# Kernel optimization log

Measured on AMD Instinct MI355X. Metric: run time of the kernel, lower is better.

Reference implementation:

```python
import jax, jax.numpy as jnp
import numpy as np

N, H, E, C, V, K = 4096, 256, 128, 32, 64, 20


def setup_inputs() -> dict:
    key = jax.random.key(0)
    ks = jax.random.split(key, 16)
    f = lambda k, s: jax.random.normal(k, s, dtype=jnp.float32)
    return {
        "vec": f(ks[0], (N, H)),
        "inp": f(ks[1], (N, E)),
        "h_prev": f(ks[2], (N, H)),
        "c_prev": f(ks[3], (N, H)),
        "Wlin": f(ks[4], (C, V, H)) * 0.05,
        "blin": f(ks[5], (C, V)) * 0.05,
        "Wec": f(ks[6], (2, H)) * 0.05,
        "bec": f(ks[7], (2,)) * 0.05,
        "Wrel": f(ks[8], (5, H)) * 0.05,
        "brel": f(ks[9], (5,)) * 0.05,
        "W_ih": f(ks[10], (K, 4 * H, E)) * 0.05,
        "b_ih": f(ks[11], (K, 4 * H)) * 0.05,
        "W_hh": f(ks[12], (K, 4 * H, H)) * 0.05,
        "b_hh": f(ks[13], (K, 4 * H)) * 0.05,
        "category": jax.random.randint(ks[14], (N,), 0, C, dtype=jnp.int32),
        "cell_id": jax.random.randint(ks[15], (N,), 0, K, dtype=jnp.int32),
        "true_idx": jax.random.randint(jax.random.fold_in(key, 100), (N,), 0, V, dtype=jnp.int32),
        "ec_idx": jax.random.randint(jax.random.fold_in(key, 101), (N,), 0, 2, dtype=jnp.int32),
        "rel_idx": jax.random.randint(jax.random.fold_in(key, 102), (N,), 0, 5, dtype=jnp.int32),
    }


def _ce(logits, targets):
    # per-row cross entropy (same math as nn.CrossEntropyLoss per example)
    logp = jax.nn.log_softmax(logits, axis=-1)
    return -jnp.take_along_axis(logp, targets[:, None], axis=-1)[:, 0]


def reference(vec, inp, h_prev, c_prev, Wlin, blin, Wec, bec, Wrel, brel,
              W_ih, b_ih, W_hh, b_hh, category, cell_id, true_idx, ec_idx, rel_idx):
    # --- get_log_odds: per-category tiny linear head, selected by category ---
    logits_all = jnp.einsum('nh,cvh->ncv', vec, Wlin) + blin          # [N,C,V]
    logits = jnp.take_along_axis(logits_all, category[:, None, None].astype(jnp.int32), axis=1)[:, 0]  # [N,V]
    logits_ec = vec @ Wec.T + bec                                      # [N,2]
    logits_rel = vec @ Wrel.T + brel                                   # [N,5]

    # --- calculate_loss: CE over valid children + ec + rel ---
    losses = _ce(logits, true_idx) + _ce(logits_ec, ec_idx) + _ce(logits_rel, rel_idx)  # [N]

    # --- get_next: per-child-index LSTMCell, selected by cell_id ---
    gates_all = (jnp.einsum('ne,kge->nkg', inp, W_ih)
                 + jnp.einsum('nh,kgh->nkg', h_prev, W_hh)
                 + b_ih + b_hh)                                        # [N,K,4H]
    gates = jnp.take_along_axis(gates_all, cell_id[:, None, None].astype(jnp.int32), axis=1)[:, 0]  # [N,4H]
    i, f, g, o = jnp.split(gates, 4, axis=-1)                          # torch LSTMCell gate order i,f,g,o
    c_next = jax.nn.sigmoid(f) * c_prev + jax.nn.sigmoid(i) * jnp.tanh(g)
    h_next = jax.nn.sigmoid(o) * jnp.tanh(c_next)

    # pack: [N, 1 + 2H] = loss | h_next | c_next
    return jnp.concatenate([losses[:, None], h_next, c_next], axis=-1)
```

## Files before the change

### kernel.cpp

```cpp
#include <hip/hip_runtime.h>
#include <hip/hip_bf16.h>
#include <math.h>

#define Nn 4096
#define Hdim 256
#define Edim 128
#define Cdim 32
#define Vdim 64
#define Kdim 20
#define G4H 1024
#define OUTS 513

#define NB 8
#define LMAX 160
#define MAXG (NB * LMAX)
#define MAXT2 192
#define GRID (MAXG + MAXT2)

typedef short bf16x8 __attribute__((ext_vector_type(8)));
typedef float f32x4 __attribute__((ext_vector_type(4)));

__device__ __forceinline__ float sigmoidf_(float x) { return 1.0f / (1.0f + expf(-x)); }

__device__ __forceinline__ bf16x8 cvt8(float4 f0, float4 f1) {
    bf16x8 r;
    __hip_bfloat16 h;
    h = __float2bfloat16(f0.x); r[0] = *(short*)&h;
    h = __float2bfloat16(f0.y); r[1] = *(short*)&h;
    h = __float2bfloat16(f0.z); r[2] = *(short*)&h;
    h = __float2bfloat16(f0.w); r[3] = *(short*)&h;
    h = __float2bfloat16(f1.x); r[4] = *(short*)&h;
    h = __float2bfloat16(f1.y); r[5] = *(short*)&h;
    h = __float2bfloat16(f1.z); r[6] = *(short*)&h;
    h = __float2bfloat16(f1.w); r[7] = *(short*)&h;
    return r;
}

__device__ __forceinline__ void gl_lds16(const float* g, void* l) {
    __builtin_amdgcn_global_load_lds((const __attribute__((address_space(1))) void*)g,
                                     (__attribute__((address_space(3))) void*)l, 16, 0, 0);
}

__global__ __launch_bounds__(256, 4) void k_all(
    const float* __restrict__ vec, const float* __restrict__ inp,
    const float* __restrict__ h_prev, const float* __restrict__ c_prev,
    const float* __restrict__ Wlin, const float* __restrict__ blin,
    const float* __restrict__ Wec, const float* __restrict__ bec,
    const float* __restrict__ Wrel, const float* __restrict__ brel,
    const float* __restrict__ W_ih, const float* __restrict__ b_ih,
    const float* __restrict__ W_hh, const float* __restrict__ b_hh,
    const int* __restrict__ category, const int* __restrict__ cell_id,
    const int* __restrict__ true_idx, const int* __restrict__ ec_idx, const int* __restrict__ rel_idx,
    float* __restrict__ out)
{
    __shared__ __align__(16) char smem[37120];
    int* rows_s = (int*)(smem + 36864);
    int* cnt  = (int*)smem;
    int* scan = (int*)(smem + 128);
    int* map  = (int*)(smem + 1152);

    int t = threadIdx.x;
    bool is_lstm = blockIdx.x < MAXG;
    const int* key = is_lstm ? cell_id : category;
    int nbins = is_lstm ? Kdim : Cdim;
    int nslots = is_lstm ? MAXG : MAXT2;
    int myslot = is_lstm ? blockIdx.x : (blockIdx.x - MAXG);

    if (t < nbins) cnt[t] = 0;
    for (int i = t; i < nslots; i += 256) map[i] = -1;
    __syncthreads();
    for (int i = t; i < Nn; i += 256) atomicAdd(&cnt[key[i]], 1);
    __syncthreads();
    if (is_lstm) {
        if (t < Kdim * 4) {
            int u = t, k = u >> 2, b = u & 7;
            int base = 0;
            for (int v = b; v < u; v += NB) base += (cnt[v >> 2] + 31) >> 5;
            int n = (cnt[k] + 31) >> 5;
            for (int s = 0; s < n; s++) {
                int slot = (base + s) * NB + b;
                if (slot < MAXG) map[slot] = u | (s << 8);
            }
        }
    } else {
        if (t < Cdim) {
            int m = t;
            int base = 0;
            for (int mm = 0; mm < m; mm++) base += (cnt[mm] + 31) >> 5;
            int n = (cnt[m] + 31) >> 5;
            for (int s = 0; s < n; s++) {
                int slot = base + s;
                if (slot < MAXT2) map[slot] = m | (s << 8);
            }
        }
    }
    __syncthreads();
    int me = map[myslot];
    if (me < 0) return;
    int myk = (me & 255);
    int s = me >> 8;
    int hb0 = 0;
    if (is_lstm) { hb0 = (myk & 3) * 64; myk >>= 2; }
    int w0 = s * 32;
    int rcount = min(32, cnt[myk] - w0);

    {
        int i0 = t * 16;
        int local = 0;
        for (int i = i0; i < i0 + 16; i++) local += (key[i] == myk) ? 1 : 0;
        scan[t] = local;
        __syncthreads();
        for (int off = 1; off < 256; off <<= 1) {
            int v = scan[t];
            int add = (t >= off) ? scan[t - off] : 0;
            __syncthreads();
            scan[t] = v + add;
            __syncthreads();
        }
        int rank = scan[t] - local;
        for (int i = i0; i < i0 + 16; i++) {
            if (key[i] == myk) {
                if (rank >= w0 && rank < w0 + 32) rows_s[rank - w0] = i;
                rank++;
            }
        }
        __syncthreads();
        if (t < 32 && t >= rcount) rows_s[t] = rows_s[0];
        __syncthreads();
    }

    int w = t >> 6, l = t & 63;
    int l15 = l & 15, quad = l >> 4;
    int lrow8 = l >> 3, lslot = l & 7;
    int swz_l = ((l15 & 3) << 1) | ((l15 >> 2) & 1);
    int p0 = (quad * 2) ^ swz_l;

    if (is_lstm) {
        float* Wbuf = (float*)smem;
        float* Xbuf = (float*)(smem + 32768);
        const float* Wih_k = W_ih + (size_t)myk * G4H * Edim;
        const float* Whh_k = W_hh + (size_t)myk * G4H * Hdim;

        f32x4 acc[2][4];
        #pragma unroll
        for (int m = 0; m < 2; m++)
            #pragma unroll
            for (int g = 0; g < 4; g++)
                acc[m][g] = (f32x4){0.f, 0.f, 0.f, 0.f};

        int xr = w * 8 + lrow8;
        int xrow = rows_s[xr];
        int xg = lslot ^ (((xr & 3) << 1) | ((xr >> 2) & 1));

        for (int st = 0; st < 12; st++) {
            int k0 = st * 32;
            const float* Wsrc; int stride, ko;
            if (k0 < Edim) { Wsrc = Wih_k; stride = Edim; ko = k0; }
            else           { Wsrc = Whh_k; stride = Hdim; ko = k0 - Edim; }
            __syncthreads();
            #pragma unroll
            for (int j = 0; j < 8; j++) {
                int r = w * 64 + j * 8 + lrow8;
                int g = lslot ^ (((r & 3) << 1) | ((r >> 2) & 1));
                int gate = r >> 6, hl = r & 63;
                gl_lds16(Wsrc + (size_t)(gate * Hdim + hb0 + hl) * stride + ko + g * 4,
                         Wbuf + (w * 64 + j * 8) * 32);
            }
            gl_lds16((k0 < Edim ? inp + (size_t)xrow * Edim + ko
                                : h_prev + (size_t)xrow * Hdim + ko) + xg * 4,
                     Xbuf + (w * 8) * 32);
            __syncthreads();

            bf16x8 af[2], bfr[4];
            #pragma unroll
            for (int m = 0; m < 2; m++) {
                int row = m * 16 + l15;
                float4 lo = *(float4*)(Xbuf + row * 32 + p0 * 4);
                float4 hi = *(float4*)(Xbuf + row * 32 + (p0 ^ 1) * 4);
                af[m] = cvt8(lo, hi);
            }
            #pragma unroll
            for (int g = 0; g < 4; g++) {
                int row = g * 64 + w * 16 + l15;
                float4 lo = *(float4*)(Wbuf + row * 32 + p0 * 4);
                float4 hi = *(float4*)(Wbuf + row * 32 + (p0 ^ 1) * 4);
                bfr[g] = cvt8(lo, hi);
            }
            #pragma unroll
            for (int m = 0; m < 2; m++)
                #pragma unroll
                for (int g = 0; g < 4; g++)
                    acc[m][g] = __builtin_amdgcn_mfma_f32_16x16x32_bf16(af[m], bfr[g], acc[m][g], 0, 0, 0);
        }

        int h = hb0 + w * 16 + l15;
        float bs[4];
        #pragma unroll
        for (int g = 0; g < 4; g++)
            bs[g] = b_ih[(size_t)myk * G4H + g * Hdim + h] + b_hh[(size_t)myk * G4H + g * Hdim + h];

        #pragma unroll
        for (int m = 0; m < 2; m++) {
            #pragma unroll
            for (int reg = 0; reg < 4; reg++) {
                int r = m * 16 + quad * 4 + reg;
                if (r < rcount) {
                    int row = rows_s[r];
                    float iv = acc[m][0][reg] + bs[0];
                    float fv = acc[m][1][reg] + bs[1];
                    float gv = acc[m][2][reg] + bs[2];
                    float ov = acc[m][3][reg] + bs[3];
                    float cp = c_prev[(size_t)row * Hdim + h];
                    float cn = sigmoidf_(fv) * cp + sigmoidf_(iv) * tanhf(gv);
                    float hn = sigmoidf_(ov) * tanhf(cn);
                    out[(size_t)row * OUTS + 1 + h] = hn;
                    out[(size_t)row * OUTS + 1 + Hdim + h] = cn;
                }
            }
        }
    } else {
        float* Wlbuf = (float*)smem;
        float* Vbuf  = (float*)(smem + 10240);
        float* Lg    = (float*)(smem + 14336);
        int m2 = myk;

        f32x4 a0[2], a1[2];
        #pragma unroll
        for (int m = 0; m < 2; m++) { a0[m] = (f32x4){0.f,0.f,0.f,0.f}; a1[m] = (f32x4){0.f,0.f,0.f,0.f}; }

        int xr = w * 8 + lrow8;
        int xrow = rows_s[xr];
        int xg = lslot ^ (((xr & 3) << 1) | ((xr >> 2) & 1));

        for (int st = 0; st < 8; st++) {
            int ko = st * 32;
            __syncthreads();
            for (int n = w; n < 10; n += 4) {
                int r = n * 8 + lrow8;
                int g = lslot ^ (((r & 3) << 1) | ((r >> 2) & 1));
                const float* srcW;
                if (r < 64)      srcW = Wlin + ((size_t)m2 * Vdim + r) * Hdim;
                else if (r < 66) srcW = Wec + (size_t)(r - 64) * Hdim;
                else if (r < 71) srcW = Wrel + (size_t)(r - 66) * Hdim;
                else             srcW = Wlin + (size_t)m2 * Vdim * Hdim;
                gl_lds16(srcW + ko + g * 4, Wlbuf + n * 8 * 32);
            }
            gl_lds16(vec + (size_t)xrow * Hdim + ko + xg * 4, Vbuf + (w * 8) * 32);
            __syncthreads();

            bf16x8 af[2];
            #pragma unroll
            for (int m = 0; m < 2; m++) {
                int row = m * 16 + l15;
                float4 lo = *(float4*)(Vbuf + row * 32 + p0 * 4);
                float4 hi = *(float4*)(Vbuf + row * 32 + (p0 ^ 1) * 4);
                af[m] = cvt8(lo, hi);
            }
            {
                int row = w * 16 + l15;
                float4 lo = *(float4*)(Wlbuf + row * 32 + p0 * 4);
                float4 hi = *(float4*)(Wlbuf + row * 32 + (p0 ^ 1) * 4);
                bf16x8 b0 = cvt8(lo, hi);
                a0[0] = __builtin_amdgcn_mfma_f32_16x16x32_bf16(af[0], b0, a0[0], 0, 0, 0);
                a0[1] = __builtin_amdgcn_mfma_f32_16x16x32_bf16(af[1], b0, a0[1], 0, 0, 0);
            }
            if (w == 3) {
                int row = 64 + l15;
                float4 lo = *(float4*)(Wlbuf + row * 32 + p0 * 4);
                float4 hi = *(float4*)(Wlbuf + row * 32 + (p0 ^ 1) * 4);
                bf16x8 b1 = cvt8(lo, hi);
                a1[0] = __builtin_amdgcn_mfma_f32_16x16x32_bf16(af[0], b1, a1[0], 0, 0, 0);
                a1[1] = __builtin_amdgcn_mfma_f32_16x16x32_bf16(af[1], b1, a1[1], 0, 0, 0);
            }
        }
        __syncthreads();
        {
            int col = w * 16 + l15;
            float bb = blin[m2 * Vdim + col];
            #pragma unroll
            for (int m = 0; m < 2; m++)
                #pragma unroll
                for (int reg = 0; reg < 4; reg++)
                    Lg[(m * 16 + quad * 4 + reg) * 84 + col] = a0[m][reg] + bb;
            if (w == 3) {
                int col1 = 64 + l15;
                float bb1 = (l15 < 2) ? bec[l15] : ((l15 < 7) ? brel[l15 - 2] : 0.f);
                #pragma unroll
                for (int m = 0; m < 2; m++)
                    #pragma unroll
                    for (int reg = 0; reg < 4; reg++)
                        Lg[(m * 16 + quad * 4 + reg) * 84 + col1] = a1[m][reg] + bb1;
            }
        }
        __syncthreads();
        for (int rr = 0; rr < 8; rr++) {
            int r = w * 8 + rr;
            if (r >= rcount) break;
            int orig = rows_s[r];
            float lg = Lg[r * 84 + l];
            float mx = lg;
            for (int ss = 32; ss >= 1; ss >>= 1) mx = fmaxf(mx, __shfl_xor(mx, ss));
            float sm = expf(lg - mx);
            for (int ss = 32; ss >= 1; ss >>= 1) sm += __shfl_xor(sm, ss);
            float lt = __shfl(lg, true_idx[orig]);
            float loss = mx + logf(sm) - lt;
            if (l == 0) {
                float l0 = Lg[r * 84 + 64], l1 = Lg[r * 84 + 65];
                float me2 = fmaxf(l0, l1);
                loss += me2 + logf(expf(l0 - me2) + expf(l1 - me2)) - ((ec_idx[orig] == 0) ? l0 : l1);
                float rl[5] = { Lg[r * 84 + 66], Lg[r * 84 + 67], Lg[r * 84 + 68], Lg[r * 84 + 69], Lg[r * 84 + 70] };
                float mr = rl[0];
                #pragma unroll
                for (int i = 1; i < 5; i++) mr = fmaxf(mr, rl[i]);
                float sr = 0.f;
                #pragma unroll
                for (int i = 0; i < 5; i++) sr += expf(rl[i] - mr);
                loss += mr + logf(sr) - rl[rel_idx[orig]];
                out[(size_t)orig * OUTS] = loss;
            }
        }
    }
}

extern "C" void kernel_launch(void* const* d_in, const int* in_sizes, int n_in,
                              void* d_out, int out_size, void* d_ws, size_t ws_size,
                              hipStream_t stream) {
    const float* vec      = (const float*)d_in[0];
    const float* inp      = (const float*)d_in[1];
    const float* h_prev   = (const float*)d_in[2];
    const float* c_prev   = (const float*)d_in[3];
    const float* Wlin     = (const float*)d_in[4];
    const float* blin     = (const float*)d_in[5];
    const float* Wec      = (const float*)d_in[6];
    const float* bec      = (const float*)d_in[7];
    const float* Wrel     = (const float*)d_in[8];
    const float* brel     = (const float*)d_in[9];
    const float* W_ih     = (const float*)d_in[10];
    const float* b_ih     = (const float*)d_in[11];
    const float* W_hh     = (const float*)d_in[12];
    const float* b_hh     = (const float*)d_in[13];
    const int*   category = (const int*)d_in[14];
    const int*   cell_id  = (const int*)d_in[15];
    const int*   true_idx = (const int*)d_in[16];
    const int*   ec_idx   = (const int*)d_in[17];
    const int*   rel_idx  = (const int*)d_in[18];
    float* out = (float*)d_out;

    k_all<<<GRID, 256, 0, stream>>>(
        vec, inp, h_prev, c_prev, Wlin, blin, Wec, bec, Wrel, brel,
        W_ih, b_ih, W_hh, b_hh, category, cell_id, true_idx, ec_idx, rel_idx, out);
}
```

Before: 156.9 us.

## Double LSTM row tile to 64 and streamline per-block binning with register keys

```diff
diff --git a/kernel.cpp b/kernel.cpp
--- a/kernel.cpp
+++ b/kernel.cpp
@@ -12,8 +12,8 @@
 #define OUTS 513
 
 #define NB 8
-#define LMAX 160
-#define MAXG (NB * LMAX)
+#define LMAXL 96
+#define MAXG (NB * LMAXL)
 #define MAXT2 192
 #define GRID (MAXG + MAXT2)
 
@@ -41,6 +41,8 @@
                                      (__attribute__((address_space(3))) void*)l, 16, 0, 0);
 }
 
+__device__ __forceinline__ int swz(int r) { return ((r & 3) << 1) | ((r >> 2) & 1); }
+
 __global__ __launch_bounds__(256, 4) void k_all(
     const float* __restrict__ vec, const float* __restrict__ inp,
     const float* __restrict__ h_prev, const float* __restrict__ c_prev,
@@ -53,86 +55,98 @@
     const int* __restrict__ true_idx, const int* __restrict__ ec_idx, const int* __restrict__ rel_idx,
     float* __restrict__ out)
 {
-    __shared__ __align__(16) char smem[37120];
-    int* rows_s = (int*)(smem + 36864);
-    int* cnt  = (int*)smem;
-    int* scan = (int*)(smem + 128);
-    int* map  = (int*)(smem + 1152);
+    __shared__ __align__(16) char smem[40960];
+    int* cntR = (int*)smem;
+    int* cntF = (int*)(smem + 8192);
+    int* wsum = (int*)(smem + 8320);
+    int* rows_tmp = (int*)(smem + 8448);
 
     int t = threadIdx.x;
+    int w = t >> 6, l = t & 63;
+    int l15 = l & 15, quad = l >> 4;
+    int lrow8 = l >> 3, lslot = l & 7;
     bool is_lstm = blockIdx.x < MAXG;
     const int* key = is_lstm ? cell_id : category;
     int nbins = is_lstm ? Kdim : Cdim;
-    int nslots = is_lstm ? MAXG : MAXT2;
-    int myslot = is_lstm ? blockIdx.x : (blockIdx.x - MAXG);
-
-    if (t < nbins) cnt[t] = 0;
-    for (int i = t; i < nslots; i += 256) map[i] = -1;
+
+    for (int i = t; i < nbins * 16; i += 256) cntR[i] = 0;
     __syncthreads();
-    for (int i = t; i < Nn; i += 256) atomicAdd(&cnt[key[i]], 1);
+    int4 kv0 = ((const int4*)key)[t * 4 + 0];
+    int4 kv1 = ((const int4*)key)[t * 4 + 1];
+    int4 kv2 = ((const int4*)key)[t * 4 + 2];
+    int4 kv3 = ((const int4*)key)[t * 4 + 3];
+    int ks[16] = { kv0.x, kv0.y, kv0.z, kv0.w, kv1.x, kv1.y, kv1.z, kv1.w,
+                   kv2.x, kv2.y, kv2.z, kv2.w, kv3.x, kv3.y, kv3.z, kv3.w };
+    int rep = t & 15;
+    #pragma unroll
+    for (int j = 0; j < 16; j++) atomicAdd(&cntR[ks[j] * 16 + rep], 1);
     __syncthreads();
-    if (is_lstm) {
-        if (t < Kdim * 4) {
-            int u = t, k = u >> 2, b = u & 7;
-            int base = 0;
-            for (int v = b; v < u; v += NB) base += (cnt[v >> 2] + 31) >> 5;
-            int n = (cnt[k] + 31) >> 5;
-            for (int s = 0; s < n; s++) {
-                int slot = (base + s) * NB + b;
-                if (slot < MAXG) map[slot] = u | (s << 8);
-            }
-        }
-    } else {
-        if (t < Cdim) {
-            int m = t;
-            int base = 0;
-            for (int mm = 0; mm < m; mm++) base += (cnt[mm] + 31) >> 5;
-            int n = (cnt[m] + 31) >> 5;
-            for (int s = 0; s < n; s++) {
-                int slot = base + s;
-                if (slot < MAXT2) map[slot] = m | (s << 8);
-            }
-        }
+    if (t < nbins) {
+        int s2 = 0;
+        #pragma unroll
+        for (int r2 = 0; r2 < 16; r2++) s2 += cntR[t * 16 + r2];
+        cntF[t] = s2;
     }
     __syncthreads();
-    int me = map[myslot];
-    if (me < 0) return;
-    int myk = (me & 255);
-    int s = me >> 8;
-    int hb0 = 0;
-    if (is_lstm) { hb0 = (myk & 3) * 64; myk >>= 2; }
-    int w0 = s * 32;
-    int rcount = min(32, cnt[myk] - w0);
+
+    int myk, s_idx, hb0 = 0, rcount, wlen;
+    if (is_lstm) {
+        int b = blockIdx.x & 7, pos = blockIdx.x >> 3;
+        int u = -1, sf = 0, acc = 0;
+        for (int uu = b; uu < Kdim * 4; uu += NB) {
+            int n = (cntF[uu >> 2] + 63) >> 6;
+            if (u < 0 && pos < acc + n) { u = uu; sf = pos - acc; }
+            acc += n;
+        }
+        if (u < 0) return;
+        myk = u >> 2; hb0 = (u & 3) * 64; s_idx = sf;
+        wlen = 64;
+        rcount = min(64, cntF[myk] - s_idx * 64);
+    } else {
+        int slot = blockIdx.x - MAXG;
+        int u = -1, sf = 0, acc = 0;
+        for (int m = 0; m < Cdim; m++) {
+            int n = (cntF[m] + 31) >> 5;
+            if (u < 0 && slot < acc + n) { u = m; sf = slot - acc; }
+            acc += n;
+        }
+        if (u < 0) return;
+        myk = u; s_idx = sf;
+        wlen = 32;
+        rcount = min(32, cntF[myk] - s_idx * 32);
+    }
 
     {
-        int i0 = t * 16;
         int local = 0;
-        for (int i = i0; i < i0 + 16; i++) local += (key[i] == myk) ? 1 : 0;
-        scan[t] = local;
-        __syncthreads();
-        for (int off = 1; off < 256; off <<= 1) {
-            int v = scan[t];
-            int add = (t >= off) ? scan[t - off] : 0;
-            __syncthreads();
-            scan[t] = v + add;
-            __syncthreads();
-        }
-        int rank = scan[t] - local;
-        for (int i = i0; i < i0 + 16; i++) {
-            if (key[i] == myk) {
-                if (rank >= w0 && rank < w0 + 32) rows_s[rank - w0] = i;
+        #pragma unroll
+        for (int j = 0; j < 16; j++) local += (ks[j] == myk) ? 1 : 0;
+        int v = local;
+        #pragma unroll
+        for (int off = 1; off < 64; off <<= 1) {
+            int n = __shfl_up(v, off);
+            if (l >= off) v += n;
+        }
+        if (l == 63) wsum[w] = v;
+        __syncthreads();
+        int wbase = 0;
+        #pragma unroll
+        for (int ww = 0; ww < 4; ww++) wbase += (ww < w) ? wsum[ww] : 0;
+        int rank = wbase + v - local;
+        int w0 = s_idx * wlen;
+        #pragma unroll
+        for (int j = 0; j < 16; j++) {
+            if (ks[j] == myk) {
+                int rr = rank - w0;
+                if (rr >= 0 && rr < wlen) rows_tmp[rr] = t * 16 + j;
                 rank++;
             }
         }
         __syncthreads();
-        if (t < 32 && t >= rcount) rows_s[t] = rows_s[0];
+        if (t < wlen && t >= rcount) rows_tmp[t] = rows_tmp[0];
         __syncthreads();
     }
-
-    int w = t >> 6, l = t & 63;
-    int l15 = l & 15, quad = l >> 4;
-    int lrow8 = l >> 3, lslot = l & 7;
-    int swz_l = ((l15 & 3) << 1) | ((l15 >> 2) & 1);
+    int reg_row = rows_tmp[is_lstm ? l : (l & 31)];
+    int swz_l = swz(l15);
     int p0 = (quad * 2) ^ swz_l;
 
     if (is_lstm) {
@@ -141,39 +155,45 @@
         const float* Wih_k = W_ih + (size_t)myk * G4H * Edim;
         const float* Whh_k = W_hh + (size_t)myk * G4H * Hdim;
 
-        f32x4 acc[2][4];
-        #pragma unroll
-        for (int m = 0; m < 2; m++)
+        int xr0 = w * 16 + lrow8;
+        int xr1 = w * 16 + 8 + lrow8;
+        int xrow0 = __shfl(reg_row, xr0);
+        int xrow1 = __shfl(reg_row, xr1);
+        int xg0 = lslot ^ swz(xr0);
+        int xg1 = lslot ^ swz(xr1);
+
+        f32x4 acc[4][4];
+        #pragma unroll
+        for (int m = 0; m < 4; m++)
             #pragma unroll
             for (int g = 0; g < 4; g++)
                 acc[m][g] = (f32x4){0.f, 0.f, 0.f, 0.f};
-
-        int xr = w * 8 + lrow8;
-        int xrow = rows_s[xr];
-        int xg = lslot ^ (((xr & 3) << 1) | ((xr >> 2) & 1));
 
         for (int st = 0; st < 12; st++) {
             int k0 = st * 32;
             const float* Wsrc; int stride, ko;
             if (k0 < Edim) { Wsrc = Wih_k; stride = Edim; ko = k0; }
             else           { Wsrc = Whh_k; stride = Hdim; ko = k0 - Edim; }
+            const float* Xs0 = (k0 < Edim) ? inp + (size_t)xrow0 * Edim + ko
+                                           : h_prev + (size_t)xrow0 * Hdim + (ko - 0);
+            const float* Xs1 = (k0 < Edim) ? inp + (size_t)xrow1 * Edim + ko
+                                           : h_prev + (size_t)xrow1 * Hdim + (ko - 0);
             __syncthreads();
             #pragma unroll
             for (int j = 0; j < 8; j++) {
                 int r = w * 64 + j * 8 + lrow8;
-                int g = lslot ^ (((r & 3) << 1) | ((r >> 2) & 1));
+                int g = lslot ^ swz(r);
                 int gate = r >> 6, hl = r & 63;
                 gl_lds16(Wsrc + (size_t)(gate * Hdim + hb0 + hl) * stride + ko + g * 4,
                          Wbuf + (w * 64 + j * 8) * 32);
             }
-            gl_lds16((k0 < Edim ? inp + (size_t)xrow * Edim + ko
-                                : h_prev + (size_t)xrow * Hdim + ko) + xg * 4,
-                     Xbuf + (w * 8) * 32);
+            gl_lds16(Xs0 + xg0 * 4, Xbuf + (w * 16) * 32);
+            gl_lds16(Xs1 + xg1 * 4, Xbuf + (w * 16 + 8) * 32);
             __syncthreads();
 
-            bf16x8 af[2], bfr[4];
-            #pragma unroll
-            for (int m = 0; m < 2; m++) {
+            bf16x8 af[4], bfr[4];
+            #pragma unroll
+            for (int m = 0; m < 4; m++) {
                 int row = m * 16 + l15;
                 float4 lo = *(float4*)(Xbuf + row * 32 + p0 * 4);
                 float4 hi = *(float4*)(Xbuf + row * 32 + (p0 ^ 1) * 4);
@@ -187,7 +207,7 @@
                 bfr[g] = cvt8(lo, hi);
             }
             #pragma unroll
-            for (int m = 0; m < 2; m++)
+            for (int m = 0; m < 4; m++)
                 #pragma unroll
                 for (int g = 0; g < 4; g++)
                     acc[m][g] = __builtin_amdgcn_mfma_f32_16x16x32_bf16(af[m], bfr[g], acc[m][g], 0, 0, 0);
@@ -200,12 +220,12 @@
             bs[g] = b_ih[(size_t)myk * G4H + g * Hdim + h] + b_hh[(size_t)myk * G4H + g * Hdim + h];
 
         #pragma unroll
-        for (int m = 0; m < 2; m++) {
+        for (int m = 0; m < 4; m++) {
             #pragma unroll
             for (int reg = 0; reg < 4; reg++) {
                 int r = m * 16 + quad * 4 + reg;
+                int row = __shfl(reg_row, r);
                 if (r < rcount) {
-                    int row = rows_s[r];
                     float iv = acc[m][0][reg] + bs[0];
                     float fv = acc[m][1][reg] + bs[1];
                     float gv = acc[m][2][reg] + bs[2];
@@ -224,20 +244,20 @@
         float* Lg    = (float*)(smem + 14336);
         int m2 = myk;
 
+        int xr = w * 8 + lrow8;
+        int xrow = __shfl(reg_row, xr);
+        int xg = lslot ^ swz(xr);
+
         f32x4 a0[2], a1[2];
         #pragma unroll
         for (int m = 0; m < 2; m++) { a0[m] = (f32x4){0.f,0.f,0.f,0.f}; a1[m] = (f32x4){0.f,0.f,0.f,0.f}; }
-
-        int xr = w * 8 + lrow8;
-        int xrow = rows_s[xr];
-        int xg = lslot ^ (((xr & 3) << 1) | ((xr >> 2) & 1));
 
         for (int st = 0; st < 8; st++) {
             int ko = st * 32;
             __syncthreads();
             for (int n = w; n < 10; n += 4) {
                 int r = n * 8 + lrow8;
-                int g = lslot ^ (((r & 3) << 1) | ((r >> 2) & 1));
+                int g = lslot ^ swz(r);
                 const float* srcW;
                 if (r < 64)      srcW = Wlin + ((size_t)m2 * Vdim + r) * Hdim;
                 else if (r < 66) srcW = Wec + (size_t)(r - 64) * Hdim;
@@ -296,7 +316,7 @@
         for (int rr = 0; rr < 8; rr++) {
             int r = w * 8 + rr;
             if (r >= rcount) break;
-            int orig = rows_s[r];
+            int orig = __shfl(reg_row, r);
             float lg = Lg[r * 84 + l];
             float mx = lg;
             for (int ss = 32; ss >= 1; ss >>= 1) mx = fmaxf(mx, __shfl_xor(mx, ss));
```

Result: no change. 154.0 us, median of 2 (-1.8%).
